# Optimization experiments

Hardware: AMD Instinct MI355X
Metric: run time of the kernel (lower is better)

## Reference

```python
import jax, jax.numpy as jnp
import numpy as np

B, T, S, A, H = 256, 256, 64, 16, 512  # batch, time, state_dim, action_dim, hypernet hidden


def setup_inputs() -> dict:
    key = jax.random.key(0)
    ks = jax.random.split(key, 12)
    x0 = jax.random.normal(ks[0], (B, S), dtype=jnp.float32)
    us = jax.random.normal(ks[1], (B, T, A), dtype=jnp.float32)
    # a_net: state_dim -> H -> S*S   (hypernetwork generating A(zx))
    Wa1 = jax.random.normal(ks[2], (S, H), dtype=jnp.float32) * 0.05
    ba1 = jax.random.normal(ks[3], (H,), dtype=jnp.float32) * 0.01
    Wa2 = jax.random.normal(ks[4], (H, S * S), dtype=jnp.float32) * 0.002  # small -> stable recurrence
    ba2 = jax.random.normal(ks[5], (S * S,), dtype=jnp.float32) * 0.002
    # b_net: action_dim -> H -> S*A  (hypernetwork generating B(zu))
    Wb1 = jax.random.normal(ks[6], (A, H), dtype=jnp.float32) * 0.05
    bb1 = jax.random.normal(ks[7], (H,), dtype=jnp.float32) * 0.01
    Wb2 = jax.random.normal(ks[8], (H, S * A), dtype=jnp.float32) * 0.02
    bb2 = jax.random.normal(ks[9], (S * A,), dtype=jnp.float32) * 0.02
    return {"x0": x0, "us": us, "Wa1": Wa1, "ba1": ba1, "Wa2": Wa2, "ba2": ba2,
            "Wb1": Wb1, "bb1": bb1, "Wb2": Wb2, "bb2": bb2}


def reference(x0, us, Wa1, ba1, Wa2, ba2, Wb1, bb1, Wb2, bb2):
    """HyperLinearSSM.rollout: x_{t+1} = A(x_t) @ x_t + B(u_t) @ u_t (zx=x, zu=u)."""
    def step(x, u):
        # hypernetwork-generated state matrix A(zx=x): [B, S, S]
        ha = jnp.tanh(x @ Wa1 + ba1)
        Amat = (ha @ Wa2 + ba2).reshape(-1, S, S)
        # hypernetwork-generated input matrix B(zu=u): [B, S, A]
        hb = jnp.tanh(u @ Wb1 + bb1)
        Bmat = (hb @ Wb2 + bb2).reshape(-1, S, A)
        x_next = jnp.einsum('bij,bj->bi', Amat, x) + jnp.einsum('bij,bj->bi', Bmat, u)
        return x_next, x_next

    us_t = jnp.transpose(us, (1, 0, 2))  # [T, B, A]
    _, xs = jax.lax.scan(step, x0, us_t)  # xs: [T, B, S]
    return jnp.transpose(xs, (1, 0, 2))   # [B, T, S]
```

## Files before the change

### kernel.cpp

```cpp
#include <hip/hip_runtime.h>

#define BSZ 256
#define TSZ 256
#define SSZ 64
#define ASZ 16
#define HSZ 512

#define NCH 16
#define HA_STR 20

#define X_OFF   0
#define HA_OFF  1024
#define W_OFF   (HA_OFF + HSZ * HA_STR)
#define RED_OFF (W_OFF + 3 * 32 * 256)
#define SMEM_FLOATS (RED_OFF + 512)
#define SMEM_BYTES  (SMEM_FLOATS * 4)

typedef float f32x4 __attribute__((ext_vector_type(4)));
typedef unsigned long long u64;

__device__ __forceinline__ void stage16(const float* gp, float* lp) {
    __builtin_amdgcn_global_load_lds(
        (const __attribute__((address_space(1))) void*)gp,
        (__attribute__((address_space(3))) void*)lp, 16, 0, 0);
}

__device__ __forceinline__ float wait_tag(const u64* p, unsigned tag) {
    u64 v = __hip_atomic_load(p, __ATOMIC_RELAXED, __HIP_MEMORY_SCOPE_AGENT);
    while ((unsigned)(v >> 32) != tag) {
        __builtin_amdgcn_s_sleep(1);
        v = __hip_atomic_load(p, __ATOMIC_RELAXED, __HIP_MEMORY_SCOPE_AGENT);
    }
    return __uint_as_float((unsigned)v);
}

__global__ __launch_bounds__(256) void bu_kernel(
    const float* __restrict__ us,
    const float* __restrict__ Wb1, const float* __restrict__ bb1,
    const float* __restrict__ Wb2, const float* __restrict__ bb2,
    float* __restrict__ out)
{
    __shared__ float u_lds[16][16];
    __shared__ float hb_lds[16][HSZ + 4];

    const int tid = threadIdx.x;
    const long s0 = (long)blockIdx.x * 16;

    u_lds[tid >> 4][tid & 15] = us[s0 * ASZ + tid];
    __syncthreads();

    #pragma unroll
    for (int rep = 0; rep < 2; ++rep) {
        const int h = tid + rep * 256;
        float acc[16];
        const float b1 = bb1[h];
        #pragma unroll
        for (int s = 0; s < 16; ++s) acc[s] = b1;
        #pragma unroll
        for (int a = 0; a < ASZ; ++a) {
            const float w = Wb1[a * HSZ + h];
            #pragma unroll
            for (int s = 0; s < 16; ++s) acc[s] += u_lds[s][a] * w;
        }
        #pragma unroll
        for (int s = 0; s < 16; ++s) hb_lds[s][h] = tanhf(acc[s]);
    }
    __syncthreads();

    const int i  = tid & 63;
    const int sg = tid >> 6;

    float ur[4][ASZ];
    #pragma unroll
    for (int s4 = 0; s4 < 4; ++s4)
        #pragma unroll
        for (int a = 0; a < ASZ; ++a) ur[s4][a] = u_lds[sg * 4 + s4][a];

    float acc[4];
    {
        float wb[ASZ];
        const float4* bp = (const float4*)(bb2 + i * ASZ);
        #pragma unroll
        for (int q = 0; q < 4; ++q) {
            float4 v = bp[q];
            wb[q*4+0] = v.x; wb[q*4+1] = v.y; wb[q*4+2] = v.z; wb[q*4+3] = v.w;
        }
        #pragma unroll
        for (int s4 = 0; s4 < 4; ++s4) {
            float t = 0.f;
            #pragma unroll
            for (int a = 0; a < ASZ; ++a) t += wb[a] * ur[s4][a];
            acc[s4] = t;
        }
    }

    for (int h = 0; h < HSZ; ++h) {
        float w[ASZ];
        const float4* wp = (const float4*)(Wb2 + (size_t)h * (SSZ * ASZ) + i * ASZ);
        #pragma unroll
        for (int q = 0; q < 4; ++q) {
            float4 v = wp[q];
            w[q*4+0] = v.x; w[q*4+1] = v.y; w[q*4+2] = v.z; w[q*4+3] = v.w;
        }
        #pragma unroll
        for (int s4 = 0; s4 < 4; ++s4) {
            float t = 0.f;
            #pragma unroll
            for (int a = 0; a < ASZ; ++a) t += w[a] * ur[s4][a];
            acc[s4] += hb_lds[sg * 4 + s4][h] * t;
        }
    }

    #pragma unroll
    for (int s4 = 0; s4 < 4; ++s4)
        out[(s0 + sg * 4 + s4) * SSZ + i] = acc[s4];
}

__global__ __launch_bounds__(512, 1) void ssm_kernel(
    const float* __restrict__ x0,
    const float* __restrict__ Wa1, const float* __restrict__ ba1,
    const float* __restrict__ Wa2, const float* __restrict__ ba2,
    float* __restrict__ out, u64* __restrict__ xbuf)
{
    extern __shared__ float smem[];
    float* x_lds = smem + X_OFF;
    float* ha_t  = smem + HA_OFF;
    float* wch   = smem + W_OFF;
    float* red   = smem + RED_OFF;

    const int tid  = threadIdx.x;
    const int lane = tid & 63;
    const int wv   = tid >> 6;
    const int bt = blockIdx.x >> 4;
    const int ct = blockIdx.x & 15;
    const long bbase = (long)bt * 16;

    const int c0 = ct * 256 + lane * 4;
    const f32x4 ba2r = *(const f32x4*)(ba2 + c0);
    const int j0 = (lane & 15) * 4;
    const int s_e = lane & 15, il_e = lane >> 4;

    for (int t = 0; t < TSZ; ++t) {
        #pragma unroll
        for (int it = 0; it < 4; ++it)
            stage16(Wa2 + (size_t)(wv * 4 + it) * 4096 + c0,
                    wch + (0 * 32 + wv * 4 + it) * 256);
        #pragma unroll
        for (int it = 0; it < 4; ++it)
            stage16(Wa2 + (size_t)(32 + wv * 4 + it) * 4096 + c0,
                    wch + (1 * 32 + wv * 4 + it) * 256);

        float bu_v = 0.f;
        if (wv == 0)
            bu_v = out[((bbase + s_e) * TSZ + t) * SSZ + (ct * 4 + il_e)];

        if (tid < 256) {
            const int sx = tid >> 4, jx = (tid & 15) * 4;
            float xv0, xv1, xv2, xv3;
            if (t > 0) {
                const u64* xs = xbuf + (size_t)((t - 1) & 3) * (BSZ * SSZ)
                              + (bbase + sx) * SSZ + jx;
                xv0 = wait_tag(xs + 0, (unsigned)t);
                xv1 = wait_tag(xs + 1, (unsigned)t);
                xv2 = wait_tag(xs + 2, (unsigned)t);
                xv3 = wait_tag(xs + 3, (unsigned)t);
            } else {
                const f32x4 x4 = *(const f32x4*)(x0 + (bbase + sx) * SSZ + jx);
                xv0 = x4.x; xv1 = x4.y; xv2 = x4.z; xv3 = x4.w;
            }
            x_lds[sx * SSZ + jx + 0] = xv0;
            x_lds[sx * SSZ + jx + 1] = xv1;
            x_lds[sx * SSZ + jx + 2] = xv2;
            x_lds[sx * SSZ + jx + 3] = xv3;
        }
        __syncthreads();

        {
            const int h0 = tid;
            float ar[16];
            const float b0 = ba1[h0];
            #pragma unroll
            for (int s = 0; s < 16; ++s) ar[s] = b0;
            #pragma unroll 4
            for (int jb = 0; jb < 16; ++jb) {
                float w0[4];
                #pragma unroll
                for (int q = 0; q < 4; ++q)
                    w0[q] = Wa1[(jb * 4 + q) * HSZ + h0];
                #pragma unroll
                for (int s = 0; s < 16; ++s) {
                    const f32x4 xr = *(const f32x4*)&x_lds[s * SSZ + jb * 4];
                    ar[s] += xr.x*w0[0] + xr.y*w0[1] + xr.z*w0[2] + xr.w*w0[3];
                }
            }
            #pragma unroll
            for (int s = 0; s < 16; ++s) ar[s] = tanhf(ar[s]);
            #pragma unroll
            for (int q = 0; q < 4; ++q) {
                f32x4 v0;
                v0.x=ar[q*4+0]; v0.y=ar[q*4+1]; v0.z=ar[q*4+2]; v0.w=ar[q*4+3];
                *(f32x4*)&ha_t[h0 * HA_STR + q * 4] = v0;
            }
        }
        __syncthreads();

        f32x4 acc[16];
        {
            const f32x4 zero = {0.f, 0.f, 0.f, 0.f};
            const f32x4 ini = (wv == 0) ? ba2r : zero;
            #pragma unroll
            for (int s = 0; s < 16; ++s) acc[s] = ini;
        }
        for (int k = 0; k < NCH; ++k) {
            if (k + 2 < NCH) {
                #pragma unroll
                for (int it = 0; it < 4; ++it)
                    stage16(Wa2 + (size_t)((k + 2) * 32 + wv * 4 + it) * 4096 + c0,
                            wch + (((k + 2) % 3) * 32 + wv * 4 + it) * 256);
                asm volatile("s_waitcnt vmcnt(8)" ::: "memory");
            } else if (k + 1 < NCH) {
                asm volatile("s_waitcnt vmcnt(4)" ::: "memory");
            } else {
                asm volatile("s_waitcnt vmcnt(0)" ::: "memory");
            }
            __builtin_amdgcn_sched_barrier(0);

            const float* wb = wch + (k % 3) * 8192 + (wv * 4) * 256;
            const float* hb = ha_t + (size_t)(k * 32 + wv * 4) * HA_STR;
            #pragma unroll
            for (int rr = 0; rr < 4; ++rr) {
                const f32x4 w4 = *(const f32x4*)(wb + rr * 256 + lane * 4);
                const f32x4 h0 = *(const f32x4*)(hb + rr * HA_STR + 0);
                const f32x4 h1 = *(const f32x4*)(hb + rr * HA_STR + 4);
                const f32x4 h2 = *(const f32x4*)(hb + rr * HA_STR + 8);
                const f32x4 h3 = *(const f32x4*)(hb + rr * HA_STR + 12);
                acc[0]  += h0.x * w4; acc[1]  += h0.y * w4;
                acc[2]  += h0.z * w4; acc[3]  += h0.w * w4;
                acc[4]  += h1.x * w4; acc[5]  += h1.y * w4;
                acc[6]  += h1.z * w4; acc[7]  += h1.w * w4;
                acc[8]  += h2.x * w4; acc[9]  += h2.y * w4;
                acc[10] += h2.z * w4; acc[11] += h2.w * w4;
                acc[12] += h3.x * w4; acc[13] += h3.y * w4;
                acc[14] += h3.z * w4; acc[15] += h3.w * w4;
            }
        }

        float part[16];
        #pragma unroll
        for (int s = 0; s < 16; ++s) {
            const f32x4 xr = *(const f32x4*)&x_lds[s * SSZ + j0];
            part[s] = acc[s].x*xr.x + acc[s].y*xr.y + acc[s].z*xr.z + acc[s].w*xr.w;
        }
        #pragma unroll
        for (int s = 0; s < 16; ++s) {
            part[s] += __shfl_xor(part[s], 1);
            part[s] += __shfl_xor(part[s], 2);
            part[s] += __shfl_xor(part[s], 4);
            part[s] += __shfl_xor(part[s], 8);
        }
        if ((lane & 15) == 0) {
            const int il = lane >> 4;
            #pragma unroll
            for (int s = 0; s < 16; ++s)
                red[(wv * 4 + il) * 16 + s] = part[s];
        }
        __syncthreads();

        if (wv == 0) {
            const long b = bbase + s_e;
            const int  i = ct * 4 + il_e;
            float r = 0.f;
            #pragma unroll
            for (int w8 = 0; w8 < 8; ++w8)
                r += red[(w8 * 4 + il_e) * 16 + s_e];
            const float xn = r + bu_v;
            out[(b * TSZ + t) * SSZ + i] = xn;
            const u64 w = ((u64)(unsigned)(t + 1) << 32)
                        | (u64)__float_as_uint(xn);
            __hip_atomic_store(xbuf + (size_t)(t & 3) * (BSZ * SSZ) + b * SSZ + i,
                               w, __ATOMIC_RELAXED, __HIP_MEMORY_SCOPE_AGENT);
        }
    }
}

extern "C" void kernel_launch(void* const* d_in, const int* in_sizes, int n_in,
                              void* d_out, int out_size, void* d_ws, size_t ws_size,
                              hipStream_t stream) {
    const float* x0  = (const float*)d_in[0];
    const float* us  = (const float*)d_in[1];
    const float* Wa1 = (const float*)d_in[2];
    const float* ba1 = (const float*)d_in[3];
    const float* Wa2 = (const float*)d_in[4];
    const float* ba2 = (const float*)d_in[5];
    const float* Wb1 = (const float*)d_in[6];
    const float* bb1 = (const float*)d_in[7];
    const float* Wb2 = (const float*)d_in[8];
    const float* bb2 = (const float*)d_in[9];
    float* out = (float*)d_out;

    u64* xbuf = (u64*)d_ws;

    hipMemsetAsync(xbuf, 0, (size_t)4 * BSZ * SSZ * sizeof(u64), stream);

    hipLaunchKernelGGL(bu_kernel, dim3((BSZ * TSZ) / 16), dim3(256), 0, stream,
                       us, Wb1, bb1, Wb2, bb2, out);

    (void)hipFuncSetAttribute((const void*)ssm_kernel,
                              hipFuncAttributeMaxDynamicSharedMemorySize, SMEM_BYTES);
    void* args[] = {(void*)&x0, (void*)&Wa1, (void*)&ba1,
                    (void*)&Wa2, (void*)&ba2, (void*)&out, (void*)&xbuf};
    hipLaunchCooperativeKernel((const void*)ssm_kernel, dim3(256), dim3(512),
                               args, SMEM_BYTES, stream);
}
```

Measured before the change: 8.241 ms.

## Use split-bf16 MFMA for the Wa2 hypernetwork GEMM in the recurrent kernel

```diff
diff --git a/kernel.cpp b/kernel.cpp
--- a/kernel.cpp
+++ b/kernel.cpp
@@ -6,9 +6,26 @@
 #define ASZ 16
 #define HSZ 512
 
+typedef float f32x4 __attribute__((ext_vector_type(4)));
+typedef short bf16x8 __attribute__((ext_vector_type(8)));
+typedef unsigned short u16x8 __attribute__((ext_vector_type(8)));
+typedef unsigned long long u64;
+typedef unsigned short ushort_t;
+
+#define XBUF_BYTES ((size_t)4 * BSZ * SSZ * sizeof(u64))
+#define WT_ELEMS   ((size_t)4096 * 512)
+#define WS_NEEDED  (XBUF_BYTES + 3 * WT_ELEMS * sizeof(ushort_t))
+
+#define MF_X_OFF    0
+#define MF_RED_OFF  4096
+#define MF_HAH_OFF  4608
+#define MF_HAM_OFF  (4608 + 16640)
+#define MF_HAL_OFF  (21248 + 16640)
+#define MF_WCH_OFF  (37888 + 16640)
+#define MF_SMEM     (54528 + 2 * 3 * 16384)
+
 #define NCH 16
 #define HA_STR 20
-
 #define X_OFF   0
 #define HA_OFF  1024
 #define W_OFF   (HA_OFF + HSZ * HA_STR)
@@ -16,10 +33,7 @@
 #define SMEM_FLOATS (RED_OFF + 512)
 #define SMEM_BYTES  (SMEM_FLOATS * 4)
 
-typedef float f32x4 __attribute__((ext_vector_type(4)));
-typedef unsigned long long u64;
-
-__device__ __forceinline__ void stage16(const float* gp, float* lp) {
+__device__ __forceinline__ void stage16(const void* gp, void* lp) {
     __builtin_amdgcn_global_load_lds(
         (const __attribute__((address_space(1))) void*)gp,
         (__attribute__((address_space(3))) void*)lp, 16, 0, 0);
@@ -32,6 +46,53 @@
         v = __hip_atomic_load(p, __ATOMIC_RELAXED, __HIP_MEMORY_SCOPE_AGENT);
     }
     return __uint_as_float((unsigned)v);
+}
+
+__device__ __forceinline__ ushort_t f32_to_bf16(float f) {
+    unsigned u = __float_as_uint(f);
+    unsigned r = u + 0x7FFFu + ((u >> 16) & 1u);
+    return (ushort_t)(r >> 16);
+}
+__device__ __forceinline__ float bf16_to_f32(ushort_t h) {
+    return __uint_as_float((unsigned)h << 16);
+}
+
+__global__ __launch_bounds__(256) void wsplit_kernel(
+    const float* __restrict__ Wa2,
+    ushort_t* __restrict__ wth, ushort_t* __restrict__ wtm,
+    ushort_t* __restrict__ wtl)
+{
+    __shared__ float tile[64][65];
+    const int bc = blockIdx.x & 63;
+    const int bh = blockIdx.x >> 6;
+    const int c0 = bc * 64, h0 = bh * 64;
+    const int tid = threadIdx.x;
+
+    const int lr = tid >> 4, lc4 = (tid & 15) * 4;
+    #pragma unroll
+    for (int p = 0; p < 4; ++p) {
+        const int h = p * 16 + lr;
+        *(f32x4*)&tile[h][lc4] =
+            *(const f32x4*)(Wa2 + (size_t)(h0 + h) * 4096 + c0 + lc4);
+    }
+    __syncthreads();
+
+    const int col = tid >> 2, hb = (tid & 3) * 16;
+    u16x8 H0, H1, M0, M1, L0, L1;
+    #pragma unroll
+    for (int q = 0; q < 16; ++q) {
+        const float v = tile[hb + q][col];
+        const ushort_t H = f32_to_bf16(v);
+        const float r1 = v - bf16_to_f32(H);
+        const ushort_t M = f32_to_bf16(r1);
+        const ushort_t L = f32_to_bf16(r1 - bf16_to_f32(M));
+        if (q < 8) { H0[q] = H; M0[q] = M; L0[q] = L; }
+        else       { H1[q-8] = H; M1[q-8] = M; L1[q-8] = L; }
+    }
+    const size_t off = (size_t)(c0 + col) * 512 + h0 + hb;
+    *(u16x8*)(wth + off) = H0;  *(u16x8*)(wth + off + 8) = H1;
+    *(u16x8*)(wtm + off) = M0;  *(u16x8*)(wtm + off + 8) = M1;
+    *(u16x8*)(wtl + off) = L0;  *(u16x8*)(wtl + off + 8) = L1;
 }
 
 __global__ __launch_bounds__(256) void bu_kernel(
@@ -116,43 +177,54 @@
         out[(s0 + sg * 4 + s4) * SSZ + i] = acc[s4];
 }
 
-__global__ __launch_bounds__(512, 1) void ssm_kernel(
+__global__ __launch_bounds__(512, 1) void ssm_mfma(
     const float* __restrict__ x0,
     const float* __restrict__ Wa1, const float* __restrict__ ba1,
-    const float* __restrict__ Wa2, const float* __restrict__ ba2,
+    const ushort_t* __restrict__ wth, const ushort_t* __restrict__ wtm,
+    const ushort_t* __restrict__ wtl, const float* __restrict__ ba2,
     float* __restrict__ out, u64* __restrict__ xbuf)
 {
-    extern __shared__ float smem[];
-    float* x_lds = smem + X_OFF;
-    float* ha_t  = smem + HA_OFF;
-    float* wch   = smem + W_OFF;
-    float* red   = smem + RED_OFF;
+    extern __shared__ char smem[];
+    float* x_lds = (float*)(smem + MF_X_OFF);
+    float* red   = (float*)(smem + MF_RED_OFF);
+    char*  haH   = smem + MF_HAH_OFF;
+    char*  haM   = smem + MF_HAM_OFF;
+    char*  haL   = smem + MF_HAL_OFF;
+    char*  wch   = smem + MF_WCH_OFF;
 
     const int tid  = threadIdx.x;
     const int lane = tid & 63;
     const int wv   = tid >> 6;
-    const int bt = blockIdx.x >> 4;
-    const int ct = blockIdx.x & 15;
+    const int l15  = lane & 15, lg = lane >> 4;
+    const int bt = blockIdx.x >> 4, ct = blockIdx.x & 15;
     const long bbase = (long)bt * 16;
 
-    const int c0 = ct * 256 + lane * 4;
-    const f32x4 ba2r = *(const f32x4*)(ba2 + c0);
-    const int j0 = (lane & 15) * 4;
-    const int s_e = lane & 15, il_e = lane >> 4;
+    const size_t wt_off = (size_t)(ct * 256 + 32 * wv + (lane >> 2)) * 512
+                        + (lane & 3) * 8;
+
+    const float ba2v0 = ba2[ct * 256 + 32 * wv + l15];
+    const float ba2v1 = ba2[ct * 256 + 32 * wv + 16 + l15];
+    const int jt  = 32 * (wv & 1) + l15;
+    const int s_e = l15, q_e = lg;
+
+    const int abyte  = l15 * 1040 + lg * 16;
+    const int b0byte = (32 * wv + l15) * 64 + lg * 16;
+    const int b1byte = b0byte + 1024;
 
     for (int t = 0; t < TSZ; ++t) {
-        #pragma unroll
-        for (int it = 0; it < 4; ++it)
-            stage16(Wa2 + (size_t)(wv * 4 + it) * 4096 + c0,
-                    wch + (0 * 32 + wv * 4 + it) * 256);
-        #pragma unroll
-        for (int it = 0; it < 4; ++it)
-            stage16(Wa2 + (size_t)(32 + wv * 4 + it) * 4096 + c0,
-                    wch + (1 * 32 + wv * 4 + it) * 256);
+        {
+            char* db = wch + 0 * 49152 + (32 * wv) * 64;
+            const ushort_t* gH = wth + wt_off;
+            const ushort_t* gM = wtm + wt_off;
+            const ushort_t* gL = wtl + wt_off;
+            stage16(gH, db);             stage16(gH + 16*512, db + 1024);
+            stage16(gM, db + 16384);     stage16(gM + 16*512, db + 16384 + 1024);
+            stage16(gL, db + 32768);     stage16(gL + 16*512, db + 32768 + 1024);
+        }
 
         float bu_v = 0.f;
         if (wv == 0)
-            bu_v = out[((bbase + s_e) * TSZ + t) * SSZ + (ct * 4 + il_e)];
+            bu_v = out[((bbase + s_e) * TSZ + t) * SSZ + (ct * 4 + q_e)];
 
         if (tid < 256) {
             const int sx = tid >> 4, jx = (tid & 15) * 4;
@@ -194,6 +266,172 @@
                 }
             }
             #pragma unroll
+            for (int s = 0; s < 16; ++s) {
+                const float v = tanhf(ar[s]);
+                const ushort_t H = f32_to_bf16(v);
+                const float r1 = v - bf16_to_f32(H);
+                const ushort_t M = f32_to_bf16(r1);
+                const ushort_t L = f32_to_bf16(r1 - bf16_to_f32(M));
+                ((ushort_t*)(haH + s * 1040))[h0] = H;
+                ((ushort_t*)(haM + s * 1040))[h0] = M;
+                ((ushort_t*)(haL + s * 1040))[h0] = L;
+            }
+        }
+        __syncthreads();
+
+        f32x4 acc0 = {0.f, 0.f, 0.f, 0.f};
+        f32x4 acc1 = {0.f, 0.f, 0.f, 0.f};
+        #pragma unroll
+        for (int k = 0; k < 16; ++k) {
+            if (k + 1 < 16) {
+                char* db = wch + ((k + 1) & 1) * 49152 + (32 * wv) * 64;
+                const ushort_t* gH = wth + wt_off + (k + 1) * 32;
+                const ushort_t* gM = wtm + wt_off + (k + 1) * 32;
+                const ushort_t* gL = wtl + wt_off + (k + 1) * 32;
+                stage16(gH, db);             stage16(gH + 16*512, db + 1024);
+                stage16(gM, db + 16384);     stage16(gM + 16*512, db + 16384 + 1024);
+                stage16(gL, db + 32768);     stage16(gL + 16*512, db + 32768 + 1024);
+                asm volatile("s_waitcnt vmcnt(6)" ::: "memory");
+            } else {
+                asm volatile("s_waitcnt vmcnt(0)" ::: "memory");
+            }
+            __builtin_amdgcn_sched_barrier(0);
+
+            const char* wb = wch + (k & 1) * 49152;
+            const bf16x8 aH  = *(const bf16x8*)(haH + k * 64 + abyte);
+            const bf16x8 aM  = *(const bf16x8*)(haM + k * 64 + abyte);
+            const bf16x8 aL  = *(const bf16x8*)(haL + k * 64 + abyte);
+            const bf16x8 b0H = *(const bf16x8*)(wb + b0byte);
+            const bf16x8 b0M = *(const bf16x8*)(wb + 16384 + b0byte);
+            const bf16x8 b0L = *(const bf16x8*)(wb + 32768 + b0byte);
+            const bf16x8 b1H = *(const bf16x8*)(wb + b1byte);
+            const bf16x8 b1M = *(const bf16x8*)(wb + 16384 + b1byte);
+            const bf16x8 b1L = *(const bf16x8*)(wb + 32768 + b1byte);
+
+            acc0 = __builtin_amdgcn_mfma_f32_16x16x32_bf16(aL, b0H, acc0, 0, 0, 0);
+            acc0 = __builtin_amdgcn_mfma_f32_16x16x32_bf16(aM, b0M, acc0, 0, 0, 0);
+            acc0 = __builtin_amdgcn_mfma_f32_16x16x32_bf16(aH, b0L, acc0, 0, 0, 0);
+            acc0 = __builtin_amdgcn_mfma_f32_16x16x32_bf16(aM, b0H, acc0, 0, 0, 0);
+            acc0 = __builtin_amdgcn_mfma_f32_16x16x32_bf16(aH, b0M, acc0, 0, 0, 0);
+            acc0 = __builtin_amdgcn_mfma_f32_16x16x32_bf16(aH, b0H, acc0, 0, 0, 0);
+            acc1 = __builtin_amdgcn_mfma_f32_16x16x32_bf16(aL, b1H, acc1, 0, 0, 0);
+            acc1 = __builtin_amdgcn_mfma_f32_16x16x32_bf16(aM, b1M, acc1, 0, 0, 0);
+            acc1 = __builtin_amdgcn_mfma_f32_16x16x32_bf16(aH, b1L, acc1, 0, 0, 0);
+            acc1 = __builtin_amdgcn_mfma_f32_16x16x32_bf16(aM, b1H, acc1, 0, 0, 0);
+            acc1 = __builtin_amdgcn_mfma_f32_16x16x32_bf16(aH, b1M, acc1, 0, 0, 0);
+            acc1 = __builtin_amdgcn_mfma_f32_16x16x32_bf16(aH, b1H, acc1, 0, 0, 0);
+        }
+
+        float part[4];
+        #pragma unroll
+        for (int r = 0; r < 4; ++r) {
+            const int s = lg * 4 + r;
+            part[r] = (acc0[r] + ba2v0) * x_lds[s * SSZ + jt]
+                    + (acc1[r] + ba2v1) * x_lds[s * SSZ + jt + 16];
+            part[r] += __shfl_xor(part[r], 1);
+            part[r] += __shfl_xor(part[r], 2);
+            part[r] += __shfl_xor(part[r], 4);
+            part[r] += __shfl_xor(part[r], 8);
+        }
+        if (l15 == 0) {
+            #pragma unroll
+            for (int r = 0; r < 4; ++r)
+                red[wv * 16 + lg * 4 + r] = part[r];
+        }
+        __syncthreads();
+
+        if (wv == 0) {
+            const long b = bbase + s_e;
+            const int  i = ct * 4 + q_e;
+            const float xn = red[(2 * q_e) * 16 + s_e]
+                           + red[(2 * q_e + 1) * 16 + s_e] + bu_v;
+            out[(b * TSZ + t) * SSZ + i] = xn;
+            const u64 w = ((u64)(unsigned)(t + 1) << 32)
+                        | (u64)__float_as_uint(xn);
+            __hip_atomic_store(xbuf + (size_t)(t & 3) * (BSZ * SSZ) + b * SSZ + i,
+                               w, __ATOMIC_RELAXED, __HIP_MEMORY_SCOPE_AGENT);
+        }
+    }
+}
+
+__global__ __launch_bounds__(512, 1) void ssm_f32(
+    const float* __restrict__ x0,
+    const float* __restrict__ Wa1, const float* __restrict__ ba1,
+    const float* __restrict__ Wa2, const float* __restrict__ ba2,
+    float* __restrict__ out, u64* __restrict__ xbuf)
+{
+    extern __shared__ float smemf[];
+    float* x_lds = smemf + X_OFF;
+    float* ha_t  = smemf + HA_OFF;
+    float* wchf  = smemf + W_OFF;
+    float* redf  = smemf + RED_OFF;
+
+    const int tid  = threadIdx.x;
+    const int lane = tid & 63;
+    const int wv   = tid >> 6;
+    const int bt = blockIdx.x >> 4;
+    const int ct = blockIdx.x & 15;
+    const long bbase = (long)bt * 16;
+
+    const int c0 = ct * 256 + lane * 4;
+    const f32x4 ba2r = *(const f32x4*)(ba2 + c0);
+    const int j0 = (lane & 15) * 4;
+    const int s_e = lane & 15, il_e = lane >> 4;
+
+    for (int t = 0; t < TSZ; ++t) {
+        #pragma unroll
+        for (int it = 0; it < 4; ++it)
+            stage16(Wa2 + (size_t)(wv * 4 + it) * 4096 + c0,
+                    wchf + (0 * 32 + wv * 4 + it) * 256);
+        #pragma unroll
+        for (int it = 0; it < 4; ++it)
+            stage16(Wa2 + (size_t)(32 + wv * 4 + it) * 4096 + c0,
+                    wchf + (1 * 32 + wv * 4 + it) * 256);
+
+        float bu_v = 0.f;
+        if (wv == 0)
+            bu_v = out[((bbase + s_e) * TSZ + t) * SSZ + (ct * 4 + il_e)];
+
+        if (tid < 256) {
+            const int sx = tid >> 4, jx = (tid & 15) * 4;
+            float xv0, xv1, xv2, xv3;
+            if (t > 0) {
+                const u64* xs = xbuf + (size_t)((t - 1) & 3) * (BSZ * SSZ)
+                              + (bbase + sx) * SSZ + jx;
+                xv0 = wait_tag(xs + 0, (unsigned)t);
+                xv1 = wait_tag(xs + 1, (unsigned)t);
+                xv2 = wait_tag(xs + 2, (unsigned)t);
+                xv3 = wait_tag(xs + 3, (unsigned)t);
+            } else {
+                const f32x4 x4 = *(const f32x4*)(x0 + (bbase + sx) * SSZ + jx);
+                xv0 = x4.x; xv1 = x4.y; xv2 = x4.z; xv3 = x4.w;
+            }
+            x_lds[sx * SSZ + jx + 0] = xv0;
+            x_lds[sx * SSZ + jx + 1] = xv1;
+            x_lds[sx * SSZ + jx + 2] = xv2;
+            x_lds[sx * SSZ + jx + 3] = xv3;
+        }
+        __syncthreads();
+
+        {
+            const int h0 = tid;
+            float ar[16];
+            const float b0 = ba1[h0];
+            #pragma unroll
+            for (int s = 0; s < 16; ++s) ar[s] = b0;
+            #pragma unroll 4
+            for (int jb = 0; jb < 16; ++jb) {
+                float w0[4];
+                #pragma unroll
+                for (int q = 0; q < 4; ++q)
+                    w0[q] = Wa1[(jb * 4 + q) * HSZ + h0];
+                #pragma unroll
+                for (int s = 0; s < 16; ++s) {
+                    const f32x4 xr = *(const f32x4*)&x_lds[s * SSZ + jb * 4];
+                    ar[s] += xr.x*w0[0] + xr.y*w0[1] + xr.z*w0[2] + xr.w*w0[3];
+                }
+            }
+            #pragma unroll
             for (int s = 0; s < 16; ++s) ar[s] = tanhf(ar[s]);
             #pragma unroll
             for (int q = 0; q < 4; ++q) {
@@ -216,7 +454,7 @@
                 #pragma unroll
                 for (int it = 0; it < 4; ++it)
                     stage16(Wa2 + (size_t)((k + 2) * 32 + wv * 4 + it) * 4096 + c0,
-                            wch + (((k + 2) % 3) * 32 + wv * 4 + it) * 256);
+                            wchf + (((k + 2) % 3) * 32 + wv * 4 + it) * 256);
                 asm volatile("s_waitcnt vmcnt(8)" ::: "memory");
             } else if (k + 1 < NCH) {
                 asm volatile("s_waitcnt vmcnt(4)" ::: "memory");
@@ -225,7 +463,7 @@
             }
             __builtin_amdgcn_sched_barrier(0);
 
-            const float* wb = wch + (k % 3) * 8192 + (wv * 4) * 256;
+            const float* wb = wchf + (k % 3) * 8192 + (wv * 4) * 256;
             const float* hb = ha_t + (size_t)(k * 32 + wv * 4) * HA_STR;
             #pragma unroll
             for (int rr = 0; rr < 4; ++rr) {
@@ -262,7 +500,7 @@
             const int il = lane >> 4;
             #pragma unroll
             for (int s = 0; s < 16; ++s)
-                red[(wv * 4 + il) * 16 + s] = part[s];
+                redf[(wv * 4 + il) * 16 + s] = part[s];
         }
         __syncthreads();
 
@@ -272,7 +510,7 @@
             float r = 0.f;
             #pragma unroll
             for (int w8 = 0; w8 < 8; ++w8)
-                r += red[(w8 * 4 + il_e) * 16 + s_e];
+                r += redf[(w8 * 4 + il_e) * 16 + s_e];
             const float xn = r + bu_v;
             out[(b * TSZ + t) * SSZ + i] = xn;
             const u64 w = ((u64)(unsigned)(t + 1) << 32)
@@ -299,16 +537,30 @@
     float* out = (float*)d_out;
 
     u64* xbuf = (u64*)d_ws;
-
-    hipMemsetAsync(xbuf, 0, (size_t)4 * BSZ * SSZ * sizeof(u64), stream);
+    hipMemsetAsync(xbuf, 0, XBUF_BYTES, stream);
 
     hipLaunchKernelGGL(bu_kernel, dim3((BSZ * TSZ) / 16), dim3(256), 0, stream,
                        us, Wb1, bb1, Wb2, bb2, out);
 
-    (void)hipFuncSetAttribute((const void*)ssm_kernel,
-                              hipFuncAttributeMaxDynamicSharedMemorySize, SMEM_BYTES);
-    void* args[] = {(void*)&x0, (void*)&Wa1, (void*)&ba1,
-                    (void*)&Wa2, (void*)&ba2, (void*)&out, (void*)&xbuf};
-    hipLaunchCooperativeKernel((const void*)ssm_kernel, dim3(256), dim3(512),
-                               args, SMEM_BYTES, stream);
-}
+    if (ws_size >= WS_NEEDED) {
+        ushort_t* wth = (ushort_t*)((char*)d_ws + XBUF_BYTES);
+        ushort_t* wtm = wth + WT_ELEMS;
+        ushort_t* wtl = wtm + WT_ELEMS;
+        hipLaunchKernelGGL(wsplit_kernel, dim3(512), dim3(256), 0, stream,
+                           Wa2, wth, wtm, wtl);
+        (void)hipFuncSetAttribute((const void*)ssm_mfma,
+                                  hipFuncAttributeMaxDynamicSharedMemorySize, MF_SMEM);
+        void* args[] = {(void*)&x0, (void*)&Wa1, (void*)&ba1,
+                        (void*)&wth, (void*)&wtm, (void*)&wtl, (void*)&ba2,
+                        (void*)&out, (void*)&xbuf};
+        hipLaunchCooperativeKernel((const void*)ssm_mfma, dim3(256), dim3(512),
+                                   args, MF_SMEM, stream);
+    } else {
+        (void)hipFuncSetAttribute((const void*)ssm_f32,
+                                  hipFuncAttributeMaxDynamicSharedMemorySize, SMEM_BYTES);
+        void* args[] = {(void*)&x0, (void*)&Wa1, (void*)&ba1,
+                        (void*)&Wa2, (void*)&ba2, (void*)&out, (void*)&xbuf};
+        hipLaunchCooperativeKernel((const void*)ssm_f32, dim3(256), dim3(512),
+                                   args, SMEM_BYTES, stream);
+    }
+}
```

Measured after the change: 8.208 ms. Within noise of the previous version (-0.4%).
